# Performance work log

Hardware: AMD Instinct MI355X
Metric: run time of the kernel (lower is better)

## Reference

```python
import jax, jax.numpy as jnp
import numpy as np

D = 1024      # features
C = 768       # context dim
H = 16        # heads
HD = D // H   # head dim = 64
N = 2048      # query tokens
M = 2048      # context tokens
EPS = 1e-12
SCALE = float(np.sqrt(HD))


def layernorm(x, w, b):
    c = x - x.mean(axis=-1, keepdims=True)
    s = (c * c).mean(axis=-1, keepdims=True)
    return c * jax.lax.rsqrt(s + EPS) * w + b


def setup_inputs() -> dict:
    key = jax.random.key(0)
    ks = jax.random.split(key, 10)
    sc = 0.02
    return {
        "x": jax.random.normal(ks[0], (N, D), jnp.float32),
        "ctx": jax.random.normal(ks[1], (M, C), jnp.float32),
        # attention projections (Projection: normal*0.02, zero bias)
        "wq": jax.random.normal(ks[2], (D, D), jnp.float32) * sc,
        "bq": jnp.zeros((D,), jnp.float32),
        "wk": jax.random.normal(ks[3], (C, D), jnp.float32) * sc,
        "bk": jnp.zeros((D,), jnp.float32),
        "wv": jax.random.normal(ks[4], (C, D), jnp.float32) * sc,
        "bv": jnp.zeros((D,), jnp.float32),
        "wo": jax.random.normal(ks[5], (D, D), jnp.float32) * sc,
        "bo": jnp.zeros((D,), jnp.float32),
        # MLP
        "w1": jax.random.normal(ks[6], (D, 4 * D), jnp.float32) * sc,
        "b1": jnp.zeros((4 * D,), jnp.float32),
        "w2": jax.random.normal(ks[7], (4 * D, D), jnp.float32) * sc,
        "b2": jnp.zeros((D,), jnp.float32),
        # layernorms
        "qn_w": jnp.ones((D,), jnp.float32), "qn_b": jnp.zeros((D,), jnp.float32),
        "kvn_w": jnp.ones((C,), jnp.float32), "kvn_b": jnp.zeros((C,), jnp.float32),
        "pn_w": jnp.ones((D,), jnp.float32), "pn_b": jnp.zeros((D,), jnp.float32),
    }


def reference(x, ctx, wq, bq, wk, bk, wv, bv, wo, bo, w1, b1, w2, b2,
              qn_w, qn_b, kvn_w, kvn_b, pn_w, pn_b):
    # pre-norm cross-attention
    xq = layernorm(x, qn_w, qn_b)          # [n, d]
    kv = layernorm(ctx, kvn_w, kvn_b)      # [m, c]
    q = (xq @ wq + bq).reshape(N, H, HD).transpose(1, 0, 2)   # [h, n, hd]
    k = (kv @ wk + bk).reshape(M, H, HD).transpose(1, 0, 2)   # [h, m, hd]
    v = (kv @ wv + bv).reshape(M, H, HD).transpose(1, 0, 2)   # [h, m, hd]
    attn = jax.nn.softmax(jnp.einsum('hnd,hmd->hnm', q, k) / SCALE, axis=-1)
    o = jnp.einsum('hnm,hmd->hnd', attn, v).transpose(1, 0, 2).reshape(N, D)
    x = (o @ wo + bo) + x
    # MLP block
    h = layernorm(x, pn_w, pn_b)
    h = jax.nn.gelu(h @ w1 + b1) @ w2 + b2
    return h + x
```

## Files before the change

### kernel.cpp

```cpp
#include <hip/hip_runtime.h>

typedef __bf16 bf16;
typedef __bf16 bf16x4 __attribute__((ext_vector_type(4)));
typedef __bf16 bf16x8 __attribute__((ext_vector_type(8)));
typedef float f32x4 __attribute__((ext_vector_type(4)));

#define N_TOK 2048
#define M_TOK 2048
#define DIM 1024
#define CDIM 768
#define DFF 4096

static __device__ __forceinline__ void async16(const void* g, void* l) {
  __builtin_amdgcn_global_load_lds((const __attribute__((address_space(1))) void*)g,
                                   (__attribute__((address_space(3))) void*)l, 16, 0, 0);
}

__device__ __forceinline__ bool detect_bf(const void* xprobe, float* sbuf) {
  int* cnt = (int*)sbuf;
  if (threadIdx.x == 0) *cnt = 0;
  __syncthreads();
  const unsigned* w = (const unsigned*)xprobe;
  int ok = 0;
  for (int i = threadIdx.x; i < 512; i += 256) {
    unsigned lo = w[i] & 0xFFFFu;
    float f = __uint_as_float(lo << 16);
    if (lo == 0u || (fabsf(f) > 1e-3f && fabsf(f) < 1e3f)) ok++;
  }
  atomicAdd(cnt, ok);
  __syncthreads();
  return *cnt >= 256;
}

__device__ __forceinline__ void t32(const void* in, bf16* out, int r0, int Rcnt,
                                    int c0, int Cfull, bool isbf, bf16* t) {
  const int cb = blockIdx.x * 32, rb = blockIdx.y * 32;
  const int tx = threadIdx.x & 31, ty = threadIdx.x >> 5;
#pragma unroll
  for (int i = 0; i < 4; i++) {
    const size_t r = (size_t)(r0 + rb + ty + i * 8);
    const size_t c = (size_t)(c0 + cb + tx);
    float v = isbf ? (float)((const bf16*)in)[r * Cfull + c]
                   : ((const float*)in)[r * Cfull + c];
    t[(ty + i * 8) * 33 + tx] = (bf16)v;
  }
  __syncthreads();
#pragma unroll
  for (int i = 0; i < 4; i++)
    out[(size_t)(cb + ty + i * 8) * Rcnt + rb + tx] = t[tx * 33 + ty + i * 8];
}

__device__ __forceinline__ void ln_row(const void* x, const void* wr, const void* br,
                                       bf16* outp, int cols, int row,
                                       bool in_bf, bool w_bf,
                                       float* xrow, float* sh) {
  const bf16* xr_b = (const bf16*)x + (size_t)row * cols;
  const float* xr_f = (const float*)x + (size_t)row * cols;
  bf16* orow = outp + (size_t)row * cols;
  float s = 0.f, ss = 0.f;
  for (int c = threadIdx.x; c < cols; c += 256) {
    float v = in_bf ? (float)xr_b[c] : xr_f[c];
    xrow[c] = v;
    s += v; ss += v * v;
  }
  for (int d = 1; d < 64; d <<= 1) { s += __shfl_xor(s, d, 64); ss += __shfl_xor(ss, d, 64); }
  const int wv = threadIdx.x >> 6, lane = threadIdx.x & 63;
  if (lane == 0) { sh[wv] = s; sh[4 + wv] = ss; }
  __syncthreads();
  s = sh[0] + sh[1] + sh[2] + sh[3];
  ss = sh[4] + sh[5] + sh[6] + sh[7];
  const float mean = s / cols;
  float var = ss / cols - mean * mean;
  var = fmaxf(var, 0.f);
  const float r = rsqrtf(var + 1e-12f);
  for (int c = threadIdx.x; c < cols; c += 256) {
    const float wv2 = w_bf ? (float)((const bf16*)wr)[c] : ((const float*)wr)[c];
    const float bv2 = w_bf ? (float)((const bf16*)br)[c] : ((const float*)br)[c];
    orow[c] = (bf16)((xrow[c] - mean) * r * wv2 + bv2);
  }
}

struct PrepArgs {
  const void* tsrc[4]; bf16* tdst[4]; int tRcnt[4], tCfull[4], tgy[4];
  const void* x; const void* qnw; const void* qnb; bf16* xq;
  const void* ctx; const void* kvnw; const void* kvnb; bf16* kvn;
  const void* csrc[12]; bf16* cdst[12]; int cn[12];
  const void* xprobe;
};
__global__ __launch_bounds__(256) void prep_kernel(PrepArgs a, int* flag) {
  __shared__ __align__(16) float sbuf[1040];
  const int z = blockIdx.z;
  const bool isbf = detect_bf(a.xprobe, sbuf);
  if (z < 4) {
    if ((int)blockIdx.y >= a.tgy[z]) return;
    t32(a.tsrc[z], a.tdst[z], 0, a.tRcnt[z], 0, a.tCfull[z], isbf, (bf16*)sbuf);
  } else if (z < 8) {
    const int row = blockIdx.x + 32 * blockIdx.y + (z & 1) * 1024;
    if (z < 6) ln_row(a.x,   a.qnw,  a.qnb,  a.xq,  DIM,  row, isbf, isbf, sbuf, sbuf + 1024);
    else       ln_row(a.ctx, a.kvnw, a.kvnb, a.kvn, CDIM, row, isbf, isbf, sbuf, sbuf + 1024);
  } else {
    const int b = blockIdx.x + 32 * blockIdx.y;
    if (b == 0 && threadIdx.x == 0) *flag = isbf ? 1 : 0;
    if (b >= 12) return;
    const void* in = a.csrc[b];
    bf16* out = a.cdst[b];
    const int n = a.cn[b];
    for (int i = threadIdx.x; i < n; i += 256)
      out[i] = isbf ? ((const bf16*)in)[i] : (bf16)((const float*)in)[i];
  }
}

struct PostArgs {
  const void* w1; bf16* w1T;
  const void* w2; bf16* w2T;
  const bf16* xat; const void* pnw; const void* pnb; bf16* hln;
};
__global__ __launch_bounds__(256) void post_kernel(PostArgs a, const int* flag) {
  __shared__ __align__(16) float sbuf[1040];
  const int z = blockIdx.z;
  const bool isbf = (*flag != 0);
  if (z == 0) {
    if (blockIdx.y >= 32) return;
    t32(a.w1, a.w1T, 0, DIM, 0, DFF, isbf, (bf16*)sbuf);
  } else if (z == 1) {
    if (blockIdx.x >= 32) return;
    t32(a.w2, a.w2T, 0, 2048, 0, DIM, isbf, (bf16*)sbuf);
  } else {
    const int row = blockIdx.x + 64 * blockIdx.y;
    if (row >= N_TOK) return;
    ln_row(a.xat, a.pnw, a.pnb, a.hln, DIM, row, true, isbf, sbuf, sbuf + 1024);
  }
}

struct TmArgs {
  const void* src[4];
  bf16* dst[4];
  int r0[4], Rcnt[4], c0[4], Cfull[4], gx[4], gy[4];
  int force_bf;
};
__global__ __launch_bounds__(256) void tmulti_kernel(TmArgs a, const int* flag) {
  const int z = blockIdx.z;
  if ((int)blockIdx.x >= a.gx[z] || (int)blockIdx.y >= a.gy[z]) return;
  __shared__ bf16 t[32 * 33];
  const bool isbf = a.force_bf || (*flag != 0);
  t32(a.src[z], a.dst[z], a.r0[z], a.Rcnt[z], a.c0[z], a.Cfull[z], isbf, t);
}

__device__ __forceinline__ float gelu_f(float x) {
  float u = 0.7978845608028654f * (x + 0.044715f * x * x * x);
  return 0.5f * x * (1.f + tanhf(u));
}

template <int EPI>
__global__ __launch_bounds__(256) void gemm64db(
    const bf16* __restrict__ A, const bf16* __restrict__ Bt,
    const bf16* __restrict__ bias, const void* __restrict__ resid,
    void* __restrict__ Cout, int K, int ldc, const int* flag) {
  __shared__ __align__(16) bf16 As[2][64 * 64];
  __shared__ __align__(16) bf16 Bs[2][64 * 64];
  const int tid = threadIdx.x;
  const int lane = tid & 63, wv = tid >> 6;
  const int lq = lane >> 4, lm = lane & 15;
  const int row0 = blockIdx.y * 64, col0 = blockIdx.x * 64;
  const int wr = (wv >> 1) * 32, wc = (wv & 1) * 32;

  const int sr = lane >> 3;
  const int sc = ((lane & 7) ^ sr) * 8;
  const int swz = (lm & 7) << 3;

  f32x4 acc[2][2] = {};

  const bf16* Abase = A + (size_t)(row0 + wv * 16 + sr) * K + sc;
  const bf16* Bbase = Bt + (size_t)(col0 + wv * 16 + sr) * K + sc;

  const int nt = K >> 6;
#pragma unroll
  for (int b = 0; b < 2; b++) {
    async16(Abase + (size_t)(b * 8) * K, &As[0][wv * 1024 + b * 512]);
    async16(Bbase + (size_t)(b * 8) * K, &Bs[0][wv * 1024 + b * 512]);
  }
  __syncthreads();

  int cur = 0;
  for (int t = 0; t < nt; ++t) {
    if (t + 1 < nt) {
      const int k1 = (t + 1) << 6;
#pragma unroll
      for (int b = 0; b < 2; b++) {
        async16(Abase + (size_t)(b * 8) * K + k1, &As[cur ^ 1][wv * 1024 + b * 512]);
        async16(Bbase + (size_t)(b * 8) * K + k1, &Bs[cur ^ 1][wv * 1024 + b * 512]);
      }
    }
#pragma unroll
    for (int kh = 0; kh < 2; kh++) {
      const int cofs = (kh * 32 + lq * 8) ^ swz;
      bf16x8 af[2], bfv[2];
#pragma unroll
      for (int i = 0; i < 2; i++)
        af[i] = *(const bf16x8*)&As[cur][(wr + i * 16 + lm) * 64 + cofs];
#pragma unroll
      for (int j = 0; j < 2; j++)
        bfv[j] = *(const bf16x8*)&Bs[cur][(wc + j * 16 + lm) * 64 + cofs];
#pragma unroll
      for (int i = 0; i < 2; i++)
#pragma unroll
        for (int j = 0; j < 2; j++)
          acc[i][j] = __builtin_amdgcn_mfma_f32_16x16x32_bf16(af[i], bfv[j], acc[i][j], 0, 0, 0);
    }
    __syncthreads();
    cur ^= 1;
  }

  const bool isbf = (*flag != 0);
#pragma unroll
  for (int i = 0; i < 2; i++) {
    const int rb = row0 + wr + i * 16 + lq * 4;
#pragma unroll
    for (int j = 0; j < 2; j++) {
      const int c = col0 + wc + j * 16 + lm;
      const float bv = (EPI != 5) ? (float)bias[c] : 0.f;
#pragma unroll
      for (int rg = 0; rg < 4; rg++) {
        const size_t idx = (size_t)(rb + rg) * ldc + c;
        float v = acc[i][j][rg] + bv;
        if (EPI == 1)
          v += isbf ? (float)((const bf16*)resid)[idx] : ((const float*)resid)[idx];
        if (EPI == 2) v = gelu_f(v);
        if (EPI == 4) v += (float)((const bf16*)resid)[idx];
        if (EPI == 5)
          v += isbf ? (float)((bf16*)Cout)[idx] : ((float*)Cout)[idx];
        if (EPI == 4 || EPI == 5) {
          if (isbf) ((bf16*)Cout)[idx] = (bf16)v;
          else      ((float*)Cout)[idx] = v;
        } else {
          ((bf16*)Cout)[idx] = (bf16)v;
        }
      }
    }
  }
}

struct QkvArgs {
  const bf16* A[3];
  const bf16* Bt[3];
  const bf16* bias[3];
  bf16* C[3];
  int K[3], ldc[3], brow[3];
};
__global__ __launch_bounds__(256) void gemm64db_qkv(QkvArgs a) {
  const int z = blockIdx.z;
  int bx, by;
  if (z < 2) { bx = blockIdx.y; by = blockIdx.x; }
  else       { bx = blockIdx.x; by = blockIdx.y; }
  const bf16* A = a.A[z];
  const bf16* Bt = a.Bt[z];
  const int K = a.K[z];
  __shared__ __align__(16) bf16 As[2][64 * 64];
  __shared__ __align__(16) bf16 Bs[2][64 * 64];
  const int tid = threadIdx.x;
  const int lane = tid & 63, wv = tid >> 6;
  const int lq = lane >> 4, lm = lane & 15;
  const int row0 = by * 64, col0 = bx * 64;
  const int wr = (wv >> 1) * 32, wc = (wv & 1) * 32;

  const int sr = lane >> 3;
  const int sc = ((lane & 7) ^ sr) * 8;
  const int swz = (lm & 7) << 3;

  f32x4 acc[2][2] = {};

  const bf16* Abase = A + (size_t)(row0 + wv * 16 + sr) * K + sc;
  const bf16* Bbase = Bt + (size_t)(col0 + wv * 16 + sr) * K + sc;

  const int nt = K >> 6;
#pragma unroll
  for (int b = 0; b < 2; b++) {
    async16(Abase + (size_t)(b * 8) * K, &As[0][wv * 1024 + b * 512]);
    async16(Bbase + (size_t)(b * 8) * K, &Bs[0][wv * 1024 + b * 512]);
  }
  __syncthreads();

  int cur = 0;
  for (int t = 0; t < nt; ++t) {
    if (t + 1 < nt) {
      const int k1 = (t + 1) << 6;
#pragma unroll
      for (int b = 0; b < 2; b++) {
        async16(Abase + (size_t)(b * 8) * K + k1, &As[cur ^ 1][wv * 1024 + b * 512]);
        async16(Bbase + (size_t)(b * 8) * K + k1, &Bs[cur ^ 1][wv * 1024 + b * 512]);
      }
    }
#pragma unroll
    for (int kh = 0; kh < 2; kh++) {
      const int cofs = (kh * 32 + lq * 8) ^ swz;
      bf16x8 af[2], bfv[2];
#pragma unroll
      for (int i = 0; i < 2; i++)
        af[i] = *(const bf16x8*)&As[cur][(wr + i * 16 + lm) * 64 + cofs];
#pragma unroll
      for (int j = 0; j < 2; j++)
        bfv[j] = *(const bf16x8*)&Bs[cur][(wc + j * 16 + lm) * 64 + cofs];
#pragma unroll
      for (int i = 0; i < 2; i++)
#pragma unroll
        for (int j = 0; j < 2; j++)
          acc[i][j] = __builtin_amdgcn_mfma_f32_16x16x32_bf16(af[i], bfv[j], acc[i][j], 0, 0, 0);
    }
    __syncthreads();
    cur ^= 1;
  }

  const bf16* bias = a.bias[z];
  bf16* C = a.C[z];
  const int ldc = a.ldc[z];
  const bool brow = a.brow[z] != 0;
#pragma unroll
  for (int i = 0; i < 2; i++) {
    const int rb = row0 + wr + i * 16 + lq * 4;
#pragma unroll
    for (int j = 0; j < 2; j++) {
      const int c = col0 + wc + j * 16 + lm;
      const float bcol = brow ? 0.f : (float)bias[c];
#pragma unroll
      for (int rg = 0; rg < 4; rg++) {
        const float bv = brow ? (float)bias[rb + rg] : bcol;
        C[(size_t)(rb + rg) * ldc + c] = (bf16)(acc[i][j][rg] + bv);
      }
    }
  }
}

__global__ __launch_bounds__(256) void attn_kernel(
    const bf16* __restrict__ q, const bf16* __restrict__ k,
    const bf16* __restrict__ vT, bf16* __restrict__ pO0, bf16* __restrict__ pO1,
    float* __restrict__ l0, float* __restrict__ l1) {
  __shared__ __align__(16) bf16 KPs[128 * 64];
  __shared__ __align__(16) bf16 Vs[64 * 128];
  const int tid = threadIdx.x, lane = tid & 63, wv = tid >> 6;
  const int lq = lane >> 4, lm = lane & 15;
  const int fid = blockIdx.x + 32 * (blockIdx.y + 16 * blockIdx.z);
  const int sid = (fid & 7) * 128 + (fid >> 3);
  const int n0 = (sid & 31) * 64;
  const int h = (sid >> 5) & 15;
  const int half = sid >> 9;
  const int mbeg = half * (M_TOK / 2), mend = mbeg + M_TOK / 2;
  bf16* pO = half ? pO1 : pO0;
  float* lb = half ? l1 : l0;

  bf16x8 qf[2];
#pragma unroll
  for (int f = 0; f < 2; f++)
    qf[f] = *(const bf16x8*)&q[(size_t)(n0 + wv * 16 + lm) * DIM + h * 64 + f * 32 + lq * 8];

  f32x4 oacc[4] = {};
  float lsum = 0.f;
  const float sc = 0.125f * 1.4426950408889634f;

  bf16x8 kreg[4], vreg[4];
#pragma unroll
  for (int it = 0; it < 4; it++) {
    const int e = tid * 8 + it * 2048;
    kreg[it] = *(const bf16x8*)&k[(size_t)(mbeg + (e >> 6)) * DIM + h * 64 + (e & 63)];
    vreg[it] = *(const bf16x8*)&vT[(size_t)(h * 64 + (e >> 7)) * M_TOK + mbeg + (e & 127)];
  }

  for (int m0 = mbeg; m0 < mend; m0 += 128) {
    asm volatile("s_waitcnt lgkmcnt(0)" ::: "memory");
    __builtin_amdgcn_s_barrier();
#pragma unroll
    for (int it = 0; it < 4; it++) {
      const int e = tid * 8 + it * 2048;
      const int kr = e >> 6, kc = e & 63;
      *(bf16x8*)&KPs[kr * 64 + (kc ^ ((kr & 7) << 3))] = kreg[it];
      const int vr = e >> 7, vc = e & 127;
      *(bf16x8*)&Vs[vr * 128 + (vc ^ ((vr & 7) << 3))] = vreg[it];
    }
    if (m0 + 128 < mend) {
      const int m1 = m0 + 128;
#pragma unroll
      for (int it = 0; it < 4; it++) {
        const int e = tid * 8 + it * 2048;
        kreg[it] = *(const bf16x8*)&k[(size_t)(m1 + (e >> 6)) * DIM + h * 64 + (e & 63)];
        vreg[it] = *(const bf16x8*)&vT[(size_t)(h * 64 + (e >> 7)) * M_TOK + m1 + (e & 127)];
      }
    }
    asm volatile("s_waitcnt lgkmcnt(0)" ::: "memory");
    __builtin_amdgcn_s_barrier();

    f32x4 s[8];
    __builtin_amdgcn_s_setprio(1);
#pragma unroll
    for (int j = 0; j < 8; j++) {
      const int kswz = (lm & 7) << 3;
      bf16x8 kf0 = *(const bf16x8*)&KPs[(j * 16 + lm) * 64 + ((lq * 8) ^ kswz)];
      bf16x8 kf1 = *(const bf16x8*)&KPs[(j * 16 + lm) * 64 + ((32 + lq * 8) ^ kswz)];
      f32x4 z = {};
      z = __builtin_amdgcn_mfma_f32_16x16x32_bf16(kf0, qf[0], z, 0, 0, 0);
      s[j] = __builtin_amdgcn_mfma_f32_16x16x32_bf16(kf1, qf[1], z, 0, 0, 0);
    }
    __builtin_amdgcn_s_setprio(0);
    asm volatile("s_waitcnt lgkmcnt(0)" ::: "memory");
    __builtin_amdgcn_s_barrier();

#pragma unroll
    for (int j = 0; j < 8; j++) {
      bf16x4 pw;
#pragma unroll
      for (int rg = 0; rg < 4; rg++) {
        const float pv = exp2f(s[j][rg] * sc);
        lsum += pv;
        pw[rg] = (bf16)pv;
      }
      *(bf16x4*)&KPs[(wv * 16 + lm) * 128 + ((j * 16 + lq * 4) ^ ((lm & 7) << 3))] = pw;
    }

    __builtin_amdgcn_s_setprio(1);
#pragma unroll
    for (int kk = 0; kk < 4; kk++) {
      bf16x8 pf = *(const bf16x8*)&KPs[(wv * 16 + lm) * 128 +
                                       ((kk * 32 + lq * 8) ^ ((lm & 7) << 3))];
#pragma unroll
      for (int dt = 0; dt < 4; dt++) {
        bf16x8 vf = *(const bf16x8*)&Vs[(dt * 16 + lm) * 128 +
                                        ((kk * 32 + lq * 8) ^ ((lm & 7) << 3))];
        oacc[dt] = __builtin_amdgcn_mfma_f32_16x16x32_bf16(vf, pf, oacc[dt], 0, 0, 0);
      }
    }
    __builtin_amdgcn_s_setprio(0);
  }

  lsum += __shfl_xor(lsum, 16, 64);
  lsum += __shfl_xor(lsum, 32, 64);
  if (lane < 16) lb[h * N_TOK + n0 + wv * 16 + lane] = lsum;

  const int rn = n0 + wv * 16 + lm;
#pragma unroll
  for (int dt = 0; dt < 4; dt++) {
    bf16x4 ow;
#pragma unroll
    for (int rg = 0; rg < 4; rg++) ow[rg] = (bf16)oacc[dt][rg];
    *(bf16x4*)&pO[(size_t)rn * DIM + h * 64 + dt * 16 + lq * 4] = ow;
  }
}

__global__ __launch_bounds__(256) void attn_combine(
    const bf16* __restrict__ pO0, const bf16* __restrict__ pO1,
    const float* __restrict__ l0, const float* __restrict__ l1,
    bf16* __restrict__ om) {
  const int i4 = (blockIdx.x * 256 + threadIdx.x) * 4;
  const int n = i4 >> 10;
  const int h = (i4 & 1023) >> 6;
  const float rinv = 1.f / (l0[h * N_TOK + n] + l1[h * N_TOK + n]);
  bf16x4 a = *(const bf16x4*)&pO0[i4];
  bf16x4 b = *(const bf16x4*)&pO1[i4];
  bf16x4 o;
#pragma unroll
  for (int r = 0; r < 4; r++) o[r] = (bf16)(((float)a[r] + (float)b[r]) * rinv);
  *(bf16x4*)&om[i4] = o;
}

extern "C" void kernel_launch(void* const* d_in, const int* in_sizes, int n_in,
                              void* d_out, int out_size, void* d_ws, size_t ws_size,
                              hipStream_t stream) {
  const void* x_r     = d_in[0];
  const void* ctx_r   = d_in[1];
  const void* wq_r    = d_in[2];
  const void* bq_r    = d_in[3];
  const void* wk_r    = d_in[4];
  const void* bk_r    = d_in[5];
  const void* wv_r    = d_in[6];
  const void* bv_r    = d_in[7];
  const void* wo_r    = d_in[8];
  const void* bo_r    = d_in[9];
  const void* w1_r    = d_in[10];
  const void* b1_r    = d_in[11];
  const void* w2_r    = d_in[12];
  const void* b2_r    = d_in[13];
  const void* qnw_r   = d_in[14];
  const void* qnb_r   = d_in[15];
  const void* kvnw_r  = d_in[16];
  const void* kvnb_r  = d_in[17];
  const void* pnw_r   = d_in[18];
  const void* pnb_r   = d_in[19];

  bf16* p = (bf16*)d_ws;
  const size_t MEG = 1024 * 1024;
  bf16* qm  = p;             bf16* hln = qm;
  bf16* km  = p + 2 * MEG;   bf16* xat = km;
  bf16* wC  = p + 4 * MEG;
  bf16* xq  = p + 8 * MEG;   bf16* pO0 = xq;   bf16* om = xq;
  bf16* vTb = p + 10 * MEG;
  bf16* kvn = p + 12 * MEG;  bf16* pO1 = kvn;
  bf16* h1h = p + 10 * MEG;
  bf16* SM  = p + 14 * MEG;
  int* flag = (int*)(p + 14 * MEG + 16384);

  bf16* wqT = wC;
  bf16* wkT = wC + 1 * MEG;
  bf16* wvT = wC + 1 * MEG + 786432;
  bf16* woT = wC + 2 * MEG + 524288;
  bf16* w1Th = wC;
  bf16* w2Th = wC + 2 * MEG;
  float* l0 = (float*)wC;
  float* l1 = l0 + N_TOK * 16;

  bf16* bqc = SM, *bkc = SM + 1024, *bvc = SM + 2048, *boc = SM + 3072;
  bf16* b1c = SM + 4096, *b2c = SM + 8192;
  bf16* qnw = SM + 9216, *qnb = SM + 10240;
  bf16* kvnw = SM + 11264, *kvnb = SM + 12032;
  bf16* pnw = SM + 12800, *pnb = SM + 13824;

  {
    PrepArgs pa;
    pa.tsrc[0] = wq_r; pa.tdst[0] = wqT; pa.tRcnt[0] = DIM;  pa.tCfull[0] = DIM; pa.tgy[0] = 32;
    pa.tsrc[1] = wk_r; pa.tdst[1] = wkT; pa.tRcnt[1] = CDIM; pa.tCfull[1] = DIM; pa.tgy[1] = 24;
    pa.tsrc[2] = wv_r; pa.tdst[2] = wvT; pa.tRcnt[2] = CDIM; pa.tCfull[2] = DIM; pa.tgy[2] = 24;
    pa.tsrc[3] = wo_r; pa.tdst[3] = woT; pa.tRcnt[3] = DIM;  pa.tCfull[3] = DIM; pa.tgy[3] = 32;
    pa.x = x_r;   pa.qnw = qnw_r;   pa.qnb = qnb_r;   pa.xq = xq;
    pa.ctx = ctx_r; pa.kvnw = kvnw_r; pa.kvnb = kvnb_r; pa.kvn = kvn;
    pa.csrc[0] = bq_r;   pa.cdst[0] = bqc;  pa.cn[0] = DIM;
    pa.csrc[1] = bk_r;   pa.cdst[1] = bkc;  pa.cn[1] = DIM;
    pa.csrc[2] = bv_r;   pa.cdst[2] = bvc;  pa.cn[2] = DIM;
    pa.csrc[3] = bo_r;   pa.cdst[3] = boc;  pa.cn[3] = DIM;
    pa.csrc[4] = b1_r;   pa.cdst[4] = b1c;  pa.cn[4] = DFF;
    pa.csrc[5] = b2_r;   pa.cdst[5] = b2c;  pa.cn[5] = DIM;
    pa.csrc[6] = qnw_r;  pa.cdst[6] = qnw;  pa.cn[6] = DIM;
    pa.csrc[7] = qnb_r;  pa.cdst[7] = qnb;  pa.cn[7] = DIM;
    pa.csrc[8] = kvnw_r; pa.cdst[8] = kvnw; pa.cn[8] = CDIM;
    pa.csrc[9] = kvnb_r; pa.cdst[9] = kvnb; pa.cn[9] = CDIM;
    pa.csrc[10] = pnw_r; pa.cdst[10] = pnw; pa.cn[10] = DIM;
    pa.csrc[11] = pnb_r; pa.cdst[11] = pnb; pa.cn[11] = DIM;
    pa.xprobe = x_r;
    prep_kernel<<<dim3(32, 32, 9), 256, 0, stream>>>(pa, flag);
  }

  {
    QkvArgs qa;
    qa.A[0] = xq;  qa.Bt[0] = wqT; qa.bias[0] = bqc; qa.C[0] = qm;
    qa.K[0] = DIM;  qa.ldc[0] = DIM;   qa.brow[0] = 0;
    qa.A[1] = kvn; qa.Bt[1] = wkT; qa.bias[1] = bkc; qa.C[1] = km;
    qa.K[1] = CDIM; qa.ldc[1] = DIM;   qa.brow[1] = 0;
    qa.A[2] = wvT; qa.Bt[2] = kvn; qa.bias[2] = bvc; qa.C[2] = vTb;
    qa.K[2] = CDIM; qa.ldc[2] = M_TOK; qa.brow[2] = 1;
    gemm64db_qkv<<<dim3(32, 16, 3), 256, 0, stream>>>(qa);
  }

  attn_kernel<<<dim3(32, 16, 2), 256, 0, stream>>>(qm, km, vTb, pO0, pO1, l0, l1);
  attn_combine<<<2048, 256, 0, stream>>>(pO0, pO1, l0, l1, om);

  gemm64db<1><<<dim3(16, 32), 256, 0, stream>>>(om, woT, boc, x_r, xat, DIM, DIM, flag);

  {
    PostArgs po;
    po.w1 = w1_r; po.w1T = w1Th;
    po.w2 = w2_r; po.w2T = w2Th;
    po.xat = xat; po.pnw = pnw_r; po.pnb = pnb_r; po.hln = hln;
    post_kernel<<<dim3(64, 64, 3), 256, 0, stream>>>(po, flag);
  }

  gemm64db<2><<<dim3(32, 32), 256, 0, stream>>>(hln, w1Th, b1c, nullptr,
                                                h1h, DIM, 2048, flag);
  gemm64db<4><<<dim3(16, 32), 256, 0, stream>>>(h1h, w2Th, b2c, xat, d_out,
                                                2048, DIM, flag);

  {
    TmArgs ta;
    ta.force_bf = 0;
    ta.src[0] = w1_r; ta.dst[0] = w1Th; ta.r0[0] = 0; ta.Rcnt[0] = DIM;
    ta.c0[0] = 2048; ta.Cfull[0] = DFF; ta.gx[0] = 64; ta.gy[0] = 32;
    ta.src[1] = w2_r; ta.dst[1] = w2Th; ta.r0[1] = 2048; ta.Rcnt[1] = 2048;
    ta.c0[1] = 0; ta.Cfull[1] = DIM; ta.gx[1] = 32; ta.gy[1] = 64;
    ta.src[2] = ta.src[0]; ta.dst[2] = ta.dst[0]; ta.r0[2] = 0; ta.Rcnt[2] = 32;
    ta.c0[2] = 0; ta.Cfull[2] = DIM; ta.gx[2] = 0; ta.gy[2] = 0;
    ta.src[3] = ta.src[0]; ta.dst[3] = ta.dst[0]; ta.r0[3] = 0; ta.Rcnt[3] = 32;
    ta.c0[3] = 0; ta.Cfull[3] = DIM; ta.gx[3] = 0; ta.gy[3] = 0;
    tmulti_kernel<<<dim3(64, 64, 2), 256, 0, stream>>>(ta, flag);
  }
  gemm64db<2><<<dim3(32, 32), 256, 0, stream>>>(hln, w1Th, b1c + 2048, nullptr,
                                                h1h, DIM, 2048, flag);
  gemm64db<5><<<dim3(16, 32), 256, 0, stream>>>(h1h, w2Th, b2c, nullptr, d_out,
                                                2048, DIM, flag);
}
```

Measured before the change: 347.1 us.

## Fuse second-half weight transposes into MLP2 GEMM and widen attention tiles

The first MLP down-projection GEMM now runs in one launch alongside the transposes of the second half of w1 and w2. The w2 half goes to a separate buffer, so it no longer waits for the GEMM that reads the first half. This removes a launch and a serial gap, and trims the post_kernel grid to drop idle blocks. The attention kernel moves to 128 query rows per block with 512 threads and a larger K/P shared tile, which halves the block count and is meant to improve K/V reuse. The cost is more shared memory per block, lower occupancy, and a new scratch buffer region whose aliasing must be safe.

```diff
diff --git a/kernel.cpp b/kernel.cpp
--- a/kernel.cpp
+++ b/kernel.cpp
@@ -32,9 +32,10 @@
   return *cnt >= 256;
 }
 
-__device__ __forceinline__ void t32(const void* in, bf16* out, int r0, int Rcnt,
-                                    int c0, int Cfull, bool isbf, bf16* t) {
-  const int cb = blockIdx.x * 32, rb = blockIdx.y * 32;
+__device__ __forceinline__ void t32(int bx, int by, const void* in, bf16* out,
+                                    int r0, int Rcnt, int c0, int Cfull,
+                                    bool isbf, bf16* t) {
+  const int cb = bx * 32, rb = by * 32;
   const int tx = threadIdx.x & 31, ty = threadIdx.x >> 5;
 #pragma unroll
   for (int i = 0; i < 4; i++) {
@@ -93,7 +94,8 @@
   const bool isbf = detect_bf(a.xprobe, sbuf);
   if (z < 4) {
     if ((int)blockIdx.y >= a.tgy[z]) return;
-    t32(a.tsrc[z], a.tdst[z], 0, a.tRcnt[z], 0, a.tCfull[z], isbf, (bf16*)sbuf);
+    t32(blockIdx.x, blockIdx.y, a.tsrc[z], a.tdst[z], 0, a.tRcnt[z], 0, a.tCfull[z],
+        isbf, (bf16*)sbuf);
   } else if (z < 8) {
     const int row = blockIdx.x + 32 * blockIdx.y + (z & 1) * 1024;
     if (z < 6) ln_row(a.x,   a.qnw,  a.qnb,  a.xq,  DIM,  row, isbf, isbf, sbuf, sbuf + 1024);
@@ -120,30 +122,14 @@
   const int z = blockIdx.z;
   const bool isbf = (*flag != 0);
   if (z == 0) {
-    if (blockIdx.y >= 32) return;
-    t32(a.w1, a.w1T, 0, DIM, 0, DFF, isbf, (bf16*)sbuf);
+    t32(blockIdx.x, blockIdx.y, a.w1, a.w1T, 0, DIM, 0, DFF, isbf, (bf16*)sbuf);
   } else if (z == 1) {
-    if (blockIdx.x >= 32) return;
-    t32(a.w2, a.w2T, 0, 2048, 0, DIM, isbf, (bf16*)sbuf);
+    const int tbx = blockIdx.x & 31, tby = blockIdx.y + 32 * (blockIdx.x >> 5);
+    t32(tbx, tby, a.w2, a.w2T, 0, 2048, 0, DIM, isbf, (bf16*)sbuf);
   } else {
     const int row = blockIdx.x + 64 * blockIdx.y;
-    if (row >= N_TOK) return;
     ln_row(a.xat, a.pnw, a.pnb, a.hln, DIM, row, true, isbf, sbuf, sbuf + 1024);
   }
-}
-
-struct TmArgs {
-  const void* src[4];
-  bf16* dst[4];
-  int r0[4], Rcnt[4], c0[4], Cfull[4], gx[4], gy[4];
-  int force_bf;
-};
-__global__ __launch_bounds__(256) void tmulti_kernel(TmArgs a, const int* flag) {
-  const int z = blockIdx.z;
-  if ((int)blockIdx.x >= a.gx[z] || (int)blockIdx.y >= a.gy[z]) return;
-  __shared__ bf16 t[32 * 33];
-  const bool isbf = a.force_bf || (*flag != 0);
-  t32(a.src[z], a.dst[z], a.r0[z], a.Rcnt[z], a.c0[z], a.Cfull[z], isbf, t);
 }
 
 __device__ __forceinline__ float gelu_f(float x) {
@@ -152,7 +138,8 @@
 }
 
 template <int EPI>
-__global__ __launch_bounds__(256) void gemm64db(
+__device__ __forceinline__ void gemm_body(
+    int bx, int by,
     const bf16* __restrict__ A, const bf16* __restrict__ Bt,
     const bf16* __restrict__ bias, const void* __restrict__ resid,
     void* __restrict__ Cout, int K, int ldc, const int* flag) {
@@ -161,7 +148,7 @@
   const int tid = threadIdx.x;
   const int lane = tid & 63, wv = tid >> 6;
   const int lq = lane >> 4, lm = lane & 15;
-  const int row0 = blockIdx.y * 64, col0 = blockIdx.x * 64;
+  const int row0 = by * 64, col0 = bx * 64;
   const int wr = (wv >> 1) * 32, wc = (wv & 1) * 32;
 
   const int sr = lane >> 3;
@@ -236,6 +223,37 @@
           ((bf16*)Cout)[idx] = (bf16)v;
         }
       }
+    }
+  }
+}
+
+template <int EPI>
+__global__ __launch_bounds__(256) void gemm64db(
+    const bf16* __restrict__ A, const bf16* __restrict__ Bt,
+    const bf16* __restrict__ bias, const void* __restrict__ resid,
+    void* __restrict__ Cout, int K, int ldc, const int* flag) {
+  gemm_body<EPI>(blockIdx.x, blockIdx.y, A, Bt, bias, resid, Cout, K, ldc, flag);
+}
+
+struct Mlp2Args {
+  const bf16* h1; const bf16* w2T; const bf16* b2; const bf16* xat; void* out;
+  const void* w1raw; bf16* w1Tdst;
+  const void* w2raw; bf16* w2Tdst;
+};
+__global__ __launch_bounds__(256) void mlp2h0_fused(Mlp2Args a, const int* flag) {
+  const int z = blockIdx.z;
+  if (z == 0) {
+    if ((int)blockIdx.x >= 16) return;
+    gemm_body<4>(blockIdx.x, blockIdx.y, a.h1, a.w2T, a.b2, a.xat, a.out,
+                 2048, DIM, flag);
+  } else {
+    __shared__ __align__(16) bf16 t[32 * 33];
+    const bool isbf = (*flag != 0);
+    if (z == 1) {
+      t32(blockIdx.x, blockIdx.y, a.w1raw, a.w1Tdst, 0, DIM, 2048, DFF, isbf, t);
+    } else {
+      const int tbx = blockIdx.x & 31, tby = blockIdx.y + 32 * (blockIdx.x >> 5);
+      t32(tbx, tby, a.w2raw, a.w2Tdst, 2048, 2048, 0, DIM, isbf, t);
     }
   }
 }
@@ -330,19 +348,19 @@
   }
 }
 
-__global__ __launch_bounds__(256) void attn_kernel(
+__global__ __launch_bounds__(512) void attn_kernel(
     const bf16* __restrict__ q, const bf16* __restrict__ k,
     const bf16* __restrict__ vT, bf16* __restrict__ pO0, bf16* __restrict__ pO1,
     float* __restrict__ l0, float* __restrict__ l1) {
-  __shared__ __align__(16) bf16 KPs[128 * 64];
+  __shared__ __align__(16) bf16 KPs[128 * 128];
   __shared__ __align__(16) bf16 Vs[64 * 128];
   const int tid = threadIdx.x, lane = tid & 63, wv = tid >> 6;
   const int lq = lane >> 4, lm = lane & 15;
-  const int fid = blockIdx.x + 32 * (blockIdx.y + 16 * blockIdx.z);
-  const int sid = (fid & 7) * 128 + (fid >> 3);
-  const int n0 = (sid & 31) * 64;
-  const int h = (sid >> 5) & 15;
-  const int half = sid >> 9;
+  const int fid = blockIdx.x + 16 * (blockIdx.y + 16 * blockIdx.z);
+  const int sid = (fid & 7) * 64 + (fid >> 3);
+  const int n0 = (sid & 15) * 128;
+  const int h = (sid >> 4) & 15;
+  const int half = sid >> 8;
   const int mbeg = half * (M_TOK / 2), mend = mbeg + M_TOK / 2;
   bf16* pO = half ? pO1 : pO0;
   float* lb = half ? l1 : l0;
@@ -356,10 +374,10 @@
   float lsum = 0.f;
   const float sc = 0.125f * 1.4426950408889634f;
 
-  bf16x8 kreg[4], vreg[4];
-#pragma unroll
-  for (int it = 0; it < 4; it++) {
-    const int e = tid * 8 + it * 2048;
+  bf16x8 kreg[2], vreg[2];
+#pragma unroll
+  for (int it = 0; it < 2; it++) {
+    const int e = tid * 8 + it * 4096;
     kreg[it] = *(const bf16x8*)&k[(size_t)(mbeg + (e >> 6)) * DIM + h * 64 + (e & 63)];
     vreg[it] = *(const bf16x8*)&vT[(size_t)(h * 64 + (e >> 7)) * M_TOK + mbeg + (e & 127)];
   }
@@ -368,8 +386,8 @@
     asm volatile("s_waitcnt lgkmcnt(0)" ::: "memory");
     __builtin_amdgcn_s_barrier();
 #pragma unroll
-    for (int it = 0; it < 4; it++) {
-      const int e = tid * 8 + it * 2048;
+    for (int it = 0; it < 2; it++) {
+      const int e = tid * 8 + it * 4096;
       const int kr = e >> 6, kc = e & 63;
       *(bf16x8*)&KPs[kr * 64 + (kc ^ ((kr & 7) << 3))] = kreg[it];
       const int vr = e >> 7, vc = e & 127;
@@ -378,8 +396,8 @@
     if (m0 + 128 < mend) {
       const int m1 = m0 + 128;
 #pragma unroll
-      for (int it = 0; it < 4; it++) {
-        const int e = tid * 8 + it * 2048;
+      for (int it = 0; it < 2; it++) {
+        const int e = tid * 8 + it * 4096;
         kreg[it] = *(const bf16x8*)&k[(size_t)(m1 + (e >> 6)) * DIM + h * 64 + (e & 63)];
         vreg[it] = *(const bf16x8*)&vT[(size_t)(h * 64 + (e >> 7)) * M_TOK + m1 + (e & 127)];
       }
@@ -501,6 +519,7 @@
   bf16* woT = wC + 2 * MEG + 524288;
   bf16* w1Th = wC;
   bf16* w2Th = wC + 2 * MEG;
+  bf16* w2Ts = p + 8 * MEG;
   float* l0 = (float*)wC;
   float* l1 = l0 + N_TOK * 16;
 
@@ -545,7 +564,7 @@
     gemm64db_qkv<<<dim3(32, 16, 3), 256, 0, stream>>>(qa);
   }
 
-  attn_kernel<<<dim3(32, 16, 2), 256, 0, stream>>>(qm, km, vTb, pO0, pO1, l0, l1);
+  attn_kernel<<<dim3(16, 16, 2), 512, 0, stream>>>(qm, km, vTb, pO0, pO1, l0, l1);
   attn_combine<<<2048, 256, 0, stream>>>(pO0, pO1, l0, l1, om);
 
   gemm64db<1><<<dim3(16, 32), 256, 0, stream>>>(om, woT, boc, x_r, xat, DIM, DIM, flag);
@@ -555,29 +574,22 @@
     po.w1 = w1_r; po.w1T = w1Th;
     po.w2 = w2_r; po.w2T = w2Th;
     po.xat = xat; po.pnw = pnw_r; po.pnb = pnb_r; po.hln = hln;
-    post_kernel<<<dim3(64, 64, 3), 256, 0, stream>>>(po, flag);
+    post_kernel<<<dim3(64, 32, 3), 256, 0, stream>>>(po, flag);
   }
 
   gemm64db<2><<<dim3(32, 32), 256, 0, stream>>>(hln, w1Th, b1c, nullptr,
                                                 h1h, DIM, 2048, flag);
-  gemm64db<4><<<dim3(16, 32), 256, 0, stream>>>(h1h, w2Th, b2c, xat, d_out,
-                                                2048, DIM, flag);
 
   {
-    TmArgs ta;
-    ta.force_bf = 0;
-    ta.src[0] = w1_r; ta.dst[0] = w1Th; ta.r0[0] = 0; ta.Rcnt[0] = DIM;
-    ta.c0[0] = 2048; ta.Cfull[0] = DFF; ta.gx[0] = 64; ta.gy[0] = 32;
-    ta.src[1] = w2_r; ta.dst[1] = w2Th; ta.r0[1] = 2048; ta.Rcnt[1] = 2048;
-    ta.c0[1] = 0; ta.Cfull[1] = DIM; ta.gx[1] = 32; ta.gy[1] = 64;
-    ta.src[2] = ta.src[0]; ta.dst[2] = ta.dst[0]; ta.r0[2] = 0; ta.Rcnt[2] = 32;
-    ta.c0[2] = 0; ta.Cfull[2] = DIM; ta.gx[2] = 0; ta.gy[2] = 0;
-    ta.src[3] = ta.src[0]; ta.dst[3] = ta.dst[0]; ta.r0[3] = 0; ta.Rcnt[3] = 32;
-    ta.c0[3] = 0; ta.Cfull[3] = DIM; ta.gx[3] = 0; ta.gy[3] = 0;
-    tmulti_kernel<<<dim3(64, 64, 2), 256, 0, stream>>>(ta, flag);
-  }
+    Mlp2Args ma;
+    ma.h1 = h1h; ma.w2T = w2Th; ma.b2 = b2c; ma.xat = xat; ma.out = d_out;
+    ma.w1raw = w1_r; ma.w1Tdst = w1Th;
+    ma.w2raw = w2_r; ma.w2Tdst = w2Ts;
+    mlp2h0_fused<<<dim3(64, 32, 3), 256, 0, stream>>>(ma, flag);
+  }
+
   gemm64db<2><<<dim3(32, 32), 256, 0, stream>>>(hln, w1Th, b1c + 2048, nullptr,
                                                 h1h, DIM, 2048, flag);
-  gemm64db<5><<<dim3(16, 32), 256, 0, stream>>>(h1h, w2Th, b2c, nullptr, d_out,
+  gemm64db<5><<<dim3(16, 32), 256, 0, stream>>>(h1h, w2Ts, b2c, nullptr, d_out,
                                                 2048, DIM, flag);
 }
```

Result: faster. 334.7 us (-3.6%).
